# Optimization experiments

Measured on AMD Instinct MI355X. Metric: run time of the kernel, lower is better.

Reference implementation:

```python
import jax, jax.numpy as jnp
import numpy as np

EPS = 1e-10
PAD = -1.0


def setup_inputs() -> dict:
    key = jax.random.key(0)
    k1, k2, k3 = jax.random.split(key, 3)
    M, N = 512, 8192
    outputs = jax.random.normal(k1, (M, N), dtype=jnp.float32)
    config_runtime = jax.random.uniform(k2, (M, N), dtype=jnp.float32)
    config_idxs = jax.random.randint(k3, (M, N), 0, 4096, dtype=jnp.int64)
    return {"outputs": outputs, "config_runtime": config_runtime, "config_idxs": config_idxs}


def _dedup_mask(config_idxs):
    # True at every occurrence of a config id except the first (by index order),
    # per row. Equivalent to the torch per-row unique/nonzero loop, vectorized
    # via a stable sort + adjacent-equal + inverse-permutation scatter.
    order = jnp.argsort(config_idxs, axis=1)            # stable sort by value
    sorted_idx = jnp.take_along_axis(config_idxs, order, axis=1)
    dup_sorted = jnp.concatenate(
        [jnp.zeros((config_idxs.shape[0], 1), dtype=bool),
         sorted_idx[:, 1:] == sorted_idx[:, :-1]], axis=1)
    inv = jnp.argsort(order, axis=1)                    # inverse permutation
    return jnp.take_along_axis(dup_sorted, inv, axis=1)


def reference(outputs, config_runtime, config_idxs):
    M, N = outputs.shape
    # 1) mark duplicate config ids as padded in y_true
    y_true = jnp.where(_dedup_mask(config_idxs), PAD, config_runtime)
    # 2) random column shuffle (torch.randperm analogue; fixed key for determinism)
    perm = jax.random.permutation(jax.random.key(42), N)
    y_pred_s = outputs[:, perm]
    y_true_s = y_true[:, perm]
    # 3) sort descending by y_true, gather preds into that order
    idx = jnp.argsort(-y_true_s, axis=1)
    y_true_sorted = jnp.take_along_axis(y_true_s, idx, axis=1)
    mask = y_true_sorted == PAD
    preds = jnp.take_along_axis(y_pred_s, idx, axis=1)
    preds = jnp.where(mask, -jnp.inf, preds)
    # 4) stable reverse-cumsum log-sum-exp
    mx = jnp.max(preds, axis=1, keepdims=True)
    pmm = jnp.where(mask, 0.0, preds - mx)              # safe: masked -> 0
    exps = jnp.where(mask, 0.0, jnp.exp(pmm))
    cums = jnp.flip(jnp.cumsum(jnp.flip(exps, axis=1), axis=1), axis=1)
    obs = jnp.where(mask, 0.0, jnp.log(cums + EPS) - pmm)
    return jnp.mean(jnp.sum(obs, axis=1))
```

## Files before the change

kernel.cpp:

```cpp
#include <hip/hip_runtime.h>
#include <hip/hip_fp16.h>

#define MROWS 512
#define NCOLS 8192
#define NVALS 4096
#define BLOCK 512
#define NW 8
#define EPSF 1e-10f

typedef unsigned int u32;
typedef unsigned long long u64;
typedef unsigned short u16;

__device__ __forceinline__ int TP(int e) { return ((e & 7) << 9) | (e >> 3); }
__device__ __forceinline__ u16 f2h(float x) { return __half_as_ushort(__float2half_rn(x)); }
__device__ __forceinline__ float h2f(u16 h) { return __half2float(__ushort_as_half(h)); }

__global__ __launch_bounds__(BLOCK, 4) void listmle_row_kernel(
    const float* __restrict__ outputs,
    const float* __restrict__ runtime,
    const int*   __restrict__ idxs,
    float* __restrict__ row_out)
{
    __shared__ u64 B[NVALS];
    __shared__ u32 A[NVALS];
    __shared__ float s_max[NW], s_ps[NW], s_fs[NW];
    __shared__ double s_lg[NW];
    __shared__ u32 s_cnt[NW];

    const int tid = threadIdx.x, lane = tid & 63, wave = tid >> 6;
    const int row = blockIdx.x;
    const float* rp = outputs + (size_t)row * NCOLS;
    const float* rr = runtime + (size_t)row * NCOLS;
    const int*   ri = idxs    + (size_t)row * NCOLS;

    u64 pk[16]; u32 pidx[8];
    float lmax = -INFINITY;
    #pragma unroll
    for (int q = 0; q < 4; ++q) {
        const int b0 = (q << 11) + (tid << 2);
        const int4   i4 = *reinterpret_cast<const int4*>(ri + b0);
        const float4 r4 = *reinterpret_cast<const float4*>(rr + b0);
        const float4 p4 = *reinterpret_cast<const float4*>(rp + b0);
        pidx[q*2]   = ((u32)i4.x & 0xFFFFu) | ((u32)i4.y << 16);
        pidx[q*2+1] = ((u32)i4.z & 0xFFFFu) | ((u32)i4.w << 16);
        const float rv[4] = { r4.x, r4.y, r4.z, r4.w };
        const float pv[4] = { p4.x, p4.y, p4.z, p4.w };
        #pragma unroll
        for (int r = 0; r < 4; ++r) {
            const int m = q*4 + r;
            u32 u = (u32)(rv[r] * 16777216.0f);
            u = u > 0xFFFFFFu ? 0xFFFFFFu : u;
            const u32 j = (u32)b0 + (u32)r;
            pk[m] = ((u64)j << 40) | ((u64)u << 16) | (u64)f2h(pv[r]);
            lmax = fmaxf(lmax, pv[r]);
        }
    }
    #pragma unroll
    for (int off = 32; off > 0; off >>= 1) lmax = fmaxf(lmax, __shfl_down(lmax, off));
    if (lane == 0) s_max[wave] = lmax;
    #pragma unroll
    for (int i = 0; i < 8; ++i) { B[(i<<9)+tid] = ~0ull; A[(i<<9)+tid] = 0u; }
    __syncthreads();

    #pragma unroll
    for (int m = 0; m < 16; ++m) {
        const u32 v = (pidx[m>>1] >> ((m & 1) << 4)) & 0xFFFFu;
        atomicMin(&B[TP((int)v)], pk[m]);
    }
    __syncthreads();

    float mx = s_max[0];
    #pragma unroll
    for (int w = 1; w < NW; ++w) mx = fmaxf(mx, s_max[w]);

    u64 own[8]; u32 keptmask = 0;
    float psum = 0.f;
    #pragma unroll
    for (int i = 0; i < 8; ++i) {
        const u64 x = B[(i<<9)+tid];
        own[i] = x;
        if (x != ~0ull) {
            keptmask |= 1u << i;
            psum += h2f((u16)(x & 0xFFFFu));
            atomicAdd(&A[TP((int)((x >> 28) & 0xFFFu))], 1u);
        }
    }
    #pragma unroll
    for (int off = 32; off > 0; off >>= 1) psum += __shfl_down(psum, off);
    if (lane == 0) s_ps[wave] = psum;
    __syncthreads();

    u32 c8[8], lsum = 0;
    #pragma unroll
    for (int i = 0; i < 8; ++i) { c8[i] = A[(i<<9)+tid]; lsum += c8[i]; }
    u32 xs = lsum;
    #pragma unroll
    for (int off = 1; off < 64; off <<= 1) { u32 y = __shfl_up(xs, off); if (lane >= off) xs += y; }
    if (lane == 63) s_cnt[wave] = xs;
    __syncthreads();

    u32 run = xs - lsum, K = 0;
    #pragma unroll
    for (int w = 0; w < NW; ++w) { const u32 t = s_cnt[w]; if (w < wave) run += t; K += t; }
    #pragma unroll
    for (int i = 0; i < 8; ++i) { const u32 c = c8[i]; A[(i<<9)+tid] = run; run += c; }
    __syncthreads();

    #pragma unroll
    for (int i = 0; i < 8; ++i) {
        if (keptmask & (1u << i)) {
            const u64 x = own[i];
            const u32 rt24 = (u32)((x >> 16) & 0xFFFFFFu);
            const u32 j    = (u32)((x >> 40) & 0x1FFFu);
            const u32 pos  = atomicAdd(&A[TP((int)(rt24 >> 12))], 1u);
            const u32 ck   = ((rt24 & 0xFFFu) << 13) | j;
            const float e  = __expf(h2f((u16)(x & 0xFFFFu)) - mx);
            B[pos] = ((u64)ck << 16) | (u64)f2h(e);
        }
    }
    __syncthreads();

    float pf[8];
    #pragma unroll
    for (int i = 0; i < 8; ++i) {
        if (keptmask & (1u << i)) {
            const u64 x = own[i];
            const u32 rt24 = (u32)((x >> 16) & 0xFFFFFFu);
            const u32 j    = (u32)((x >> 40) & 0x1FFFu);
            const int b    = (int)(rt24 >> 12);
            const u32 start = b ? A[TP(b - 1)] : 0u;
            const u32 end   = A[TP(b)];
            const u32 ck    = ((rt24 & 0xFFFu) << 13) | j;
            double dsm = 0.0;
            for (u32 q = start; q < end; ++q) {
                const u64 v = B[q];
                if ((u32)(v >> 16) <= ck) dsm += (double)h2f((u16)(v & 0xFFFFu));
            }
            pf[i] = (float)dsm;
        }
    }
    float f8[8];
    {
        u32 st = tid ? A[TP(8 * tid - 1)] : 0u;
        #pragma unroll
        for (int i = 0; i < 8; ++i) {
            const u32 end = A[(i<<9)+tid];
            double ds = 0.0;
            for (u32 q = st; q < end; ++q) ds += (double)h2f((u16)(B[q] & 0xFFFFu));
            f8[i] = (float)ds;
            st = end;
        }
    }
    float fsum = 0.f;
    #pragma unroll
    for (int i = 0; i < 8; ++i) fsum += f8[i];
    float xf = fsum;
    #pragma unroll
    for (int off = 1; off < 64; off <<= 1) { const float y = __shfl_up(xf, off); if (lane >= off) xf += y; }
    if (lane == 63) s_fs[wave] = xf;
    __syncthreads();

    float Tx = xf - fsum;
    #pragma unroll
    for (int w = 0; w < NW; ++w) if (w < wave) Tx += s_fs[w];
    #pragma unroll
    for (int i = 0; i < 8; ++i) { A[(i<<9)+tid] = __float_as_uint(Tx); Tx += f8[i]; }
    __syncthreads();

    double logacc = 0.0;
    #pragma unroll
    for (int i = 0; i < 8; ++i) {
        if (keptmask & (1u << i)) {
            const int b = (int)((own[i] >> 28) & 0xFFFu);
            const float S = __uint_as_float(A[TP(b)]);
            logacc += (double)__logf(S + pf[i] + EPSF);
        }
    }
    #pragma unroll
    for (int off = 32; off > 0; off >>= 1) logacc += __shfl_down(logacc, off);
    if (lane == 0) s_lg[wave] = logacc;
    __syncthreads();

    if (tid == 0) {
        double lt = 0.0; float pt = 0.f;
        #pragma unroll
        for (int w = 0; w < NW; ++w) { lt += s_lg[w]; pt += s_ps[w]; }
        row_out[row] = (float)(lt - (double)pt + (double)((float)K * mx));
    }
}

__global__ __launch_bounds__(256) void listmle_finalize(
    const float* __restrict__ row_out, float* __restrict__ out)
{
    __shared__ double red_d[4];
    const int tid = threadIdx.x;
    const int lane = tid & 63, wave = tid >> 6;
    double acc = 0.0;
    for (int r = tid; r < MROWS; r += 256) acc += (double)row_out[r];
    #pragma unroll
    for (int off = 32; off > 0; off >>= 1) acc += __shfl_down(acc, off);
    if (lane == 0) red_d[wave] = acc;
    __syncthreads();
    if (tid == 0) {
        double tot = 0.0;
        for (int w = 0; w < 4; ++w) tot += red_d[w];
        out[0] = (float)(tot / (double)MROWS);
    }
}

extern "C" void kernel_launch(void* const* d_in, const int* in_sizes, int n_in,
                              void* d_out, int out_size, void* d_ws, size_t ws_size,
                              hipStream_t stream) {
    const float* outputs = (const float*)d_in[0];
    const float* runtime = (const float*)d_in[1];
    const int*   idxs    = (const int*)d_in[2];
    float* out = (float*)d_out;
    float* ws  = (float*)d_ws;

    listmle_row_kernel<<<MROWS, BLOCK, 0, stream>>>(outputs, runtime, idxs, ws);
    listmle_finalize<<<1, 256, 0, stream>>>(ws, out);
}
```

Before: 27.18 us.

## Fuse bucket counts and fixed-point exp sums into one packed 64-bit scan

Each bucket now accumulates a single 64-bit word holding the element count in the upper 20 bits and a fixed-point sum of exp values in the lower 44 bits. One prefix scan then yields both the scatter offsets and the suffix-sum bases, which removes the second scan, its barriers and the per-thread range re-summing pass. Scatter positions are transposed for bank-friendly access, and the in-bucket partial sums are computed per slot instead of per owner. The cost is extra LDS (a 64-bit D array) with launch bounds lowered to 2 blocks per SM, and a fixed-point quantization of the exp values.

```diff
diff --git a/kernel.cpp b/kernel.cpp
--- a/kernel.cpp
+++ b/kernel.cpp
@@ -12,21 +12,27 @@
 typedef unsigned long long u64;
 typedef unsigned short u16;
 
+#define TOTMASK ((1ull << 44) - 1ull)
+#define FXSCALE 1073741824.0f
+
 __device__ __forceinline__ int TP(int e) { return ((e & 7) << 9) | (e >> 3); }
 __device__ __forceinline__ u16 f2h(float x) { return __half_as_ushort(__float2half_rn(x)); }
 __device__ __forceinline__ float h2f(u16 h) { return __half2float(__ushort_as_half(h)); }
 
-__global__ __launch_bounds__(BLOCK, 4) void listmle_row_kernel(
+__global__ __launch_bounds__(BLOCK, 2) void listmle_row_kernel(
     const float* __restrict__ outputs,
     const float* __restrict__ runtime,
     const int*   __restrict__ idxs,
     float* __restrict__ row_out)
 {
     __shared__ u64 B[NVALS];
-    __shared__ u32 A[NVALS];
-    __shared__ float s_max[NW], s_ps[NW], s_fs[NW];
+    __shared__ u64 D[NVALS];
+    __shared__ u64 s_sc[NW];
+    __shared__ float s_max[NW], s_ps[NW];
     __shared__ double s_lg[NW];
-    __shared__ u32 s_cnt[NW];
+
+    u32* Cc = reinterpret_cast<u32*>(D);
+    u32* Sf = reinterpret_cast<u32*>(D) + NVALS;
 
     const int tid = threadIdx.x, lane = tid & 63, wave = tid >> 6;
     const int row = blockIdx.x;
@@ -48,11 +54,10 @@
         const float pv[4] = { p4.x, p4.y, p4.z, p4.w };
         #pragma unroll
         for (int r = 0; r < 4; ++r) {
-            const int m = q*4 + r;
             u32 u = (u32)(rv[r] * 16777216.0f);
             u = u > 0xFFFFFFu ? 0xFFFFFFu : u;
             const u32 j = (u32)b0 + (u32)r;
-            pk[m] = ((u64)j << 40) | ((u64)u << 16) | (u64)f2h(pv[r]);
+            pk[q*4+r] = ((u64)j << 40) | ((u64)u << 16) | (u64)f2h(pv[r]);
             lmax = fmaxf(lmax, pv[r]);
         }
     }
@@ -60,7 +65,7 @@
     for (int off = 32; off > 0; off >>= 1) lmax = fmaxf(lmax, __shfl_down(lmax, off));
     if (lane == 0) s_max[wave] = lmax;
     #pragma unroll
-    for (int i = 0; i < 8; ++i) { B[(i<<9)+tid] = ~0ull; A[(i<<9)+tid] = 0u; }
+    for (int i = 0; i < 8; ++i) { B[(i<<9)+tid] = ~0ull; D[(i<<9)+tid] = 0ull; }
     __syncthreads();
 
     #pragma unroll
@@ -74,7 +79,8 @@
     #pragma unroll
     for (int w = 1; w < NW; ++w) mx = fmaxf(mx, s_max[w]);
 
-    u64 own[8]; u32 keptmask = 0;
+    u64 own[8]; float e8[8];
+    u32 keptmask = 0;
     float psum = 0.f;
     #pragma unroll
     for (int i = 0; i < 8; ++i) {
@@ -82,8 +88,12 @@
         own[i] = x;
         if (x != ~0ull) {
             keptmask |= 1u << i;
-            psum += h2f((u16)(x & 0xFFFFu));
-            atomicAdd(&A[TP((int)((x >> 28) & 0xFFFu))], 1u);
+            const float pd = h2f((u16)(x & 0xFFFFu));
+            psum += pd;
+            const float e = __expf(pd - mx);
+            e8[i] = e;
+            const int b = (int)((x >> 28) & 0xFFFu);
+            atomicAdd(&D[TP(b)], (1ull << 44) | (u64)(e * FXSCALE + 0.5f));
         }
     }
     #pragma unroll
@@ -91,20 +101,25 @@
     if (lane == 0) s_ps[wave] = psum;
     __syncthreads();
 
-    u32 c8[8], lsum = 0;
+    u64 d8[8], lsum = 0ull;
     #pragma unroll
-    for (int i = 0; i < 8; ++i) { c8[i] = A[(i<<9)+tid]; lsum += c8[i]; }
-    u32 xs = lsum;
+    for (int i = 0; i < 8; ++i) { d8[i] = D[(i<<9)+tid]; lsum += d8[i]; }
+    u64 xsu = lsum;
     #pragma unroll
-    for (int off = 1; off < 64; off <<= 1) { u32 y = __shfl_up(xs, off); if (lane >= off) xs += y; }
-    if (lane == 63) s_cnt[wave] = xs;
+    for (int off = 1; off < 64; off <<= 1) { const u64 y = __shfl_up(xsu, off); if (lane >= off) xsu += y; }
+    if (lane == 63) s_sc[wave] = xsu;
     __syncthreads();
 
-    u32 run = xs - lsum, K = 0;
+    u64 runp = xsu - lsum, grand = 0ull;
     #pragma unroll
-    for (int w = 0; w < NW; ++w) { const u32 t = s_cnt[w]; if (w < wave) run += t; K += t; }
+    for (int w = 0; w < NW; ++w) { const u64 t = s_sc[w]; if (w < wave) runp += t; grand += t; }
+    const u32 K = (u32)(grand >> 44);
     #pragma unroll
-    for (int i = 0; i < 8; ++i) { const u32 c = c8[i]; A[(i<<9)+tid] = run; run += c; }
+    for (int i = 0; i < 8; ++i) {
+        Cc[(i<<9)+tid] = (u32)(runp >> 44);
+        Sf[(i<<9)+tid] = __float_as_uint((float)(runp & TOTMASK) * (1.0f / FXSCALE));
+        runp += d8[i];
+    }
     __syncthreads();
 
     #pragma unroll
@@ -113,68 +128,29 @@
             const u64 x = own[i];
             const u32 rt24 = (u32)((x >> 16) & 0xFFFFFFu);
             const u32 j    = (u32)((x >> 40) & 0x1FFFu);
-            const u32 pos  = atomicAdd(&A[TP((int)(rt24 >> 12))], 1u);
-            const u32 ck   = ((rt24 & 0xFFFu) << 13) | j;
-            const float e  = __expf(h2f((u16)(x & 0xFFFFu)) - mx);
-            B[pos] = ((u64)ck << 16) | (u64)f2h(e);
+            const u32 pos  = atomicAdd(&Cc[TP((int)(rt24 >> 12))], 1u);
+            B[TP((int)pos)] = ((u64)rt24 << 29) | ((u64)j << 16) | (u64)f2h(e8[i]);
         }
     }
-    __syncthreads();
-
-    float pf[8];
-    #pragma unroll
-    for (int i = 0; i < 8; ++i) {
-        if (keptmask & (1u << i)) {
-            const u64 x = own[i];
-            const u32 rt24 = (u32)((x >> 16) & 0xFFFFFFu);
-            const u32 j    = (u32)((x >> 40) & 0x1FFFu);
-            const int b    = (int)(rt24 >> 12);
-            const u32 start = b ? A[TP(b - 1)] : 0u;
-            const u32 end   = A[TP(b)];
-            const u32 ck    = ((rt24 & 0xFFFu) << 13) | j;
-            double dsm = 0.0;
-            for (u32 q = start; q < end; ++q) {
-                const u64 v = B[q];
-                if ((u32)(v >> 16) <= ck) dsm += (double)h2f((u16)(v & 0xFFFFu));
-            }
-            pf[i] = (float)dsm;
-        }
-    }
-    float f8[8];
-    {
-        u32 st = tid ? A[TP(8 * tid - 1)] : 0u;
-        #pragma unroll
-        for (int i = 0; i < 8; ++i) {
-            const u32 end = A[(i<<9)+tid];
-            double ds = 0.0;
-            for (u32 q = st; q < end; ++q) ds += (double)h2f((u16)(B[q] & 0xFFFFu));
-            f8[i] = (float)ds;
-            st = end;
-        }
-    }
-    float fsum = 0.f;
-    #pragma unroll
-    for (int i = 0; i < 8; ++i) fsum += f8[i];
-    float xf = fsum;
-    #pragma unroll
-    for (int off = 1; off < 64; off <<= 1) { const float y = __shfl_up(xf, off); if (lane >= off) xf += y; }
-    if (lane == 63) s_fs[wave] = xf;
-    __syncthreads();
-
-    float Tx = xf - fsum;
-    #pragma unroll
-    for (int w = 0; w < NW; ++w) if (w < wave) Tx += s_fs[w];
-    #pragma unroll
-    for (int i = 0; i < 8; ++i) { A[(i<<9)+tid] = __float_as_uint(Tx); Tx += f8[i]; }
     __syncthreads();
 
     double logacc = 0.0;
     #pragma unroll
     for (int i = 0; i < 8; ++i) {
-        if (keptmask & (1u << i)) {
-            const int b = (int)((own[i] >> 28) & 0xFFFu);
-            const float S = __uint_as_float(A[TP(b)]);
-            logacc += (double)__logf(S + pf[i] + EPSF);
+        const u32 p = (u32)(8 * tid + i);
+        if (p < K) {
+            const u64 x = B[(i<<9)+tid];
+            const u64 ku = x >> 16;
+            const int b  = (int)(x >> 41);
+            const u32 start = b ? Cc[TP(b - 1)] : 0u;
+            const u32 end   = Cc[TP(b)];
+            double dsm = 0.0;
+            for (u32 q = start; q < end; ++q) {
+                const u64 y = B[TP((int)q)];
+                if ((y >> 16) <= ku) dsm += (double)h2f((u16)(y & 0xFFFFu));
+            }
+            const float S = __uint_as_float(Sf[TP(b)]);
+            logacc += (double)__logf(S + (float)dsm + EPSF);
         }
     }
     #pragma unroll
```

Result: no change. 26.86 us (-1.2%).
